# Kernel optimization log

Measured on AMD Instinct MI355X. Metric: run time of the kernel, lower is better.

Reference implementation:

```python
import jax, jax.numpy as jnp
import numpy as np

B, S, D, H = 1, 2048, 2048, 16
NOPE, ROPE, VH = 128, 64, 128
QK = NOPE + ROPE
QLORA, KVLORA = 1536, 512


def rms_norm(x, w, eps=1e-6):
    xf = x.astype(jnp.float32)
    y = xf * jax.lax.rsqrt(jnp.mean(xf * xf, axis=-1, keepdims=True) + eps)
    return (w * y).astype(x.dtype)


def apply_rope(x, cos, sin):
    # x: [b, s, h, d]; cos/sin: [s, d/2]; complex mult on consecutive pairs
    x2 = x.reshape(*x.shape[:-1], -1, 2)
    x0, x1 = x2[..., 0], x2[..., 1]
    c = cos[None, :, None, :]
    s = sin[None, :, None, :]
    y0 = x0 * c - x1 * s
    y1 = x0 * s + x1 * c
    return jnp.stack([y0, y1], axis=-1).reshape(x.shape).astype(x.dtype)


def setup_inputs() -> dict:
    key = jax.random.key(0)
    ks = jax.random.split(key, 8)
    init = lambda k, shape, fan: (jax.random.normal(k, shape, jnp.float32) / np.sqrt(fan))
    x = jax.random.normal(ks[0], (B, S, D), jnp.float32)
    wq_down_w = init(ks[1], (QLORA, D), D)
    wq_down_b = jnp.zeros((QLORA,), jnp.float32)
    q_norm_w = jnp.ones((QLORA,), jnp.float32)
    wq_up_w = init(ks[2], (H * QK, QLORA), QLORA)
    wq_up_b = jnp.zeros((H * QK,), jnp.float32)
    wkv_down_w = init(ks[3], (KVLORA + ROPE, D), D)
    wkv_down_b = jnp.zeros((KVLORA + ROPE,), jnp.float32)
    kv_norm_w = jnp.ones((KVLORA,), jnp.float32)
    wkv_up_w = init(ks[4], (H * (NOPE + VH), KVLORA), KVLORA)
    wkv_up_b = jnp.zeros((H * (NOPE + VH),), jnp.float32)
    wo_w = init(ks[5], (D, H * VH), H * VH)
    wo_b = jnp.zeros((D,), jnp.float32)
    pos = jnp.arange(S, dtype=jnp.float32)
    inv = 1.0 / (10000.0 ** (jnp.arange(0, ROPE, 2, dtype=jnp.float32) / ROPE))
    ang = pos[:, None] * inv[None, :]  # [S, ROPE/2]
    freqs_cos, freqs_sin = jnp.cos(ang), jnp.sin(ang)
    causal = jnp.tril(jnp.ones((S, S), bool))
    mask = jnp.broadcast_to(jnp.where(causal, 0.0, -1e9).astype(jnp.float32), (B, S, S))
    return dict(x=x, start_pos=0, freqs_cos=freqs_cos, freqs_sin=freqs_sin, mask=mask,
                wq_down_w=wq_down_w, wq_down_b=wq_down_b, q_norm_w=q_norm_w,
                wq_up_w=wq_up_w, wq_up_b=wq_up_b,
                wkv_down_w=wkv_down_w, wkv_down_b=wkv_down_b, kv_norm_w=kv_norm_w,
                wkv_up_w=wkv_up_w, wkv_up_b=wkv_up_b, wo_w=wo_w, wo_b=wo_b)


def reference(x, start_pos, freqs_cos, freqs_sin, mask,
              wq_down_w, wq_down_b, q_norm_w, wq_up_w, wq_up_b,
              wkv_down_w, wkv_down_b, kv_norm_w, wkv_up_w, wkv_up_b,
              wo_w, wo_b):
    bsz, seqlen, _ = x.shape
    scale = QK ** (-0.5)
    # low-rank query path
    q = rms_norm(x @ wq_down_w.T + wq_down_b, q_norm_w)
    q = (q @ wq_up_w.T + wq_up_b).reshape(bsz, seqlen, H, QK)
    q_nope, q_pe = q[..., :NOPE], q[..., NOPE:]
    q_pe = apply_rope(q_pe, freqs_cos, freqs_sin)
    # low-rank kv path with decoupled rope key
    kv = x @ wkv_down_w.T + wkv_down_b
    kv_lat, k_pe = kv[..., :KVLORA], kv[..., KVLORA:]
    kv_up = rms_norm(kv_lat, kv_norm_w) @ wkv_up_w.T + wkv_up_b
    kv_up = kv_up.reshape(bsz, seqlen, H, NOPE + VH)
    k_nope, v = kv_up[..., :NOPE], kv_up[..., NOPE:]
    k_pe = apply_rope(k_pe[:, :, None, :], freqs_cos, freqs_sin)  # [b,s,1,ROPE]
    qf = jnp.concatenate([q_nope, q_pe], axis=-1)
    kf = jnp.concatenate([k_nope, jnp.broadcast_to(k_pe, (bsz, seqlen, H, ROPE))], axis=-1)
    scores = jnp.einsum('bqhd,bkhd->bhqk', qf, kf) * scale
    scores = scores + mask[:, None, :, :]
    probs = jax.nn.softmax(scores.astype(jnp.float32), axis=-1).astype(x.dtype)
    out = jnp.einsum('bhqk,bkhd->bqhd', probs, v).reshape(bsz, seqlen, H * VH)
    return out @ wo_w.T + wo_b
```

## Files before the change

### kernel.cpp

```cpp
#include <hip/hip_runtime.h>
#include <math.h>

typedef __attribute__((ext_vector_type(8))) __bf16 bf16x8;
typedef __attribute__((ext_vector_type(8))) short short8;
typedef __attribute__((ext_vector_type(4))) float f32x4;
typedef __attribute__((ext_vector_type(4))) unsigned short u16x4;

#define S_LEN 2048
#define NHEAD 16

__device__ __forceinline__ unsigned short f2b(float f) {
    unsigned int u = __float_as_uint(f);
    u = (u + 0x7fffu + ((u >> 16) & 1u)) >> 16;
    return (unsigned short)u;
}

__device__ __forceinline__ f32x4 mfma16(short8 a, short8 b, f32x4 c) {
    return __builtin_amdgcn_mfma_f32_16x16x32_bf16(
        __builtin_bit_cast(bf16x8, a), __builtin_bit_cast(bf16x8, b), c, 0, 0, 0);
}

#define GLDS(gptr, lptr)                                                              \
    __builtin_amdgcn_global_load_lds(                                                 \
        (const __attribute__((address_space(1))) unsigned int*)(gptr),                \
        (__attribute__((address_space(3))) unsigned int*)(lptr), 16, 0, 0)

__global__ __launch_bounds__(256) void cvt_f2b(const float* __restrict__ in,
                                               unsigned short* __restrict__ out, int n4) {
    int i = blockIdx.x * 256 + threadIdx.x;
    if (i >= n4) return;
    float4 v = ((const float4*)in)[i];
    u16x4 o;
    o[0] = f2b(v.x); o[1] = f2b(v.y); o[2] = f2b(v.z); o[3] = f2b(v.w);
    ((u16x4*)out)[i] = o;
}

__global__ __launch_bounds__(256) void cvt_f2b_pad(const float* __restrict__ in,
                                                   unsigned short* __restrict__ out,
                                                   int N, int K, int Npad) {
    int i = blockIdx.x * 256 + threadIdx.x;
    int total4 = Npad * (K >> 2);
    if (i >= total4) return;
    int r = (i * 4) / K;
    u16x4 o = {0, 0, 0, 0};
    if (r < N) {
        float4 v = ((const float4*)in)[i];
        o[0] = f2b(v.x); o[1] = f2b(v.y); o[2] = f2b(v.z); o[3] = f2b(v.w);
    }
    ((u16x4*)out)[i] = o;
}

__global__ __launch_bounds__(256) void gemm_bt(const unsigned short* __restrict__ A,
                                               const unsigned short* __restrict__ W,
                                               const float* __restrict__ bias,
                                               float* __restrict__ C,
                                               int M, int N, int K, int Npad,
                                               int tiles_m) {
    __shared__ __align__(16) unsigned short sA[128 * 32];
    __shared__ __align__(16) unsigned short sB[128 * 32];
    const int tid = threadIdx.x;
    const int wave = tid >> 6, lane = tid & 63;
    const int l15 = lane & 15, l4 = lane >> 4;
    const int wm = wave >> 1, wn = wave & 1;

    const int nwg = gridDim.x;
    const int q8 = nwg >> 3, r8 = nwg & 7;
    const int xcd = blockIdx.x & 7, ii = blockIdx.x >> 3;
    const int sw = ((xcd < r8) ? xcd * (q8 + 1) : r8 * (q8 + 1) + (xcd - r8) * q8) + ii;
    const int bm = sw % tiles_m, bn = sw / tiles_m;

    f32x4 acc[4][4] = {};
    const int nkt = K >> 5;
    for (int kt = 0; kt < nkt; ++kt) {
#pragma unroll
        for (int j = 0; j < 2; ++j) {
            int cbase = (j * 4 + wave) * 64;
            int c = cbase + lane;
            int r = c >> 2, c8 = c & 3;
            GLDS(&A[(size_t)(bm * 128 + r) * K + kt * 32 + c8 * 8],
                 (char*)sA + cbase * 16);
            GLDS(&W[(size_t)(bn * 128 + r) * K + kt * 32 + c8 * 8],
                 (char*)sB + cbase * 16);
        }
        __syncthreads();
        short8 af[4], bf[4];
#pragma unroll
        for (int mi = 0; mi < 4; ++mi)
            af[mi] = *(const short8*)&sA[(wm * 64 + mi * 16 + l15) * 32 + 8 * l4];
#pragma unroll
        for (int ni = 0; ni < 4; ++ni)
            bf[ni] = *(const short8*)&sB[(wn * 64 + ni * 16 + l15) * 32 + 8 * l4];
#pragma unroll
        for (int mi = 0; mi < 4; ++mi)
#pragma unroll
            for (int ni = 0; ni < 4; ++ni)
                acc[mi][ni] = mfma16(af[mi], bf[ni], acc[mi][ni]);
        __syncthreads();
    }
#pragma unroll
    for (int mi = 0; mi < 4; ++mi) {
        int row = bm * 128 + wm * 64 + mi * 16 + 4 * l4;
#pragma unroll
        for (int ni = 0; ni < 4; ++ni) {
            int col = bn * 128 + wn * 64 + ni * 16 + l15;
            float b = (col < N) ? bias[col] : 0.f;
#pragma unroll
            for (int r = 0; r < 4; ++r)
                C[(size_t)(row + r) * Npad + col] = acc[mi][ni][r] + b;
        }
    }
}

__global__ __launch_bounds__(256) void rmsnorm_k(const float* __restrict__ in,
                                                 const float* __restrict__ w,
                                                 unsigned short* __restrict__ out,
                                                 int K, int ldin) {
    int row = blockIdx.x, tid = threadIdx.x;
    const float* p = in + (size_t)row * ldin;
    float ss = 0.f;
    for (int i = tid; i < K; i += 256) { float v = p[i]; ss += v * v; }
#pragma unroll
    for (int off = 1; off < 64; off <<= 1) ss += __shfl_xor(ss, off, 64);
    __shared__ float red[4];
    if ((tid & 63) == 0) red[tid >> 6] = ss;
    __syncthreads();
    float tot = red[0] + red[1] + red[2] + red[3];
    float rinv = rsqrtf(tot / (float)K + 1e-6f);
    for (int i = tid; i < K; i += 256)
        out[(size_t)row * K + i] = f2b(p[i] * rinv * w[i]);
}

__global__ __launch_bounds__(256) void assemble_q(const float* __restrict__ qup,
                                                  const float* __restrict__ fcos,
                                                  const float* __restrict__ fsin,
                                                  unsigned short* __restrict__ qf) {
    int s = blockIdx.x, tid = threadIdx.x;
    const float scale = 0.07216878365f;
    for (int idx = tid; idx < NHEAD * 128; idx += 256) {
        int h = idx >> 7, j = idx & 127;
        qf[((size_t)h * S_LEN + s) * 192 + j] = f2b(qup[(size_t)s * 3072 + h * 192 + j] * scale);
    }
    for (int idx = tid; idx < NHEAD * 32; idx += 256) {
        int h = idx >> 5, j = idx & 31;
        float x0 = qup[(size_t)s * 3072 + h * 192 + 128 + 2 * j];
        float x1 = qup[(size_t)s * 3072 + h * 192 + 128 + 2 * j + 1];
        float c = fcos[s * 32 + j], sn = fsin[s * 32 + j];
        size_t base = ((size_t)h * S_LEN + s) * 192 + 128 + 2 * j;
        qf[base]     = f2b((x0 * c - x1 * sn) * scale);
        qf[base + 1] = f2b((x0 * sn + x1 * c) * scale);
    }
}

__global__ __launch_bounds__(256) void assemble_k(const float* __restrict__ kvup,
                                                  const float* __restrict__ kvd,
                                                  const float* __restrict__ fcos,
                                                  const float* __restrict__ fsin,
                                                  unsigned short* __restrict__ kf) {
    int s = blockIdx.x, tid = threadIdx.x;
    __shared__ unsigned short pe[64];
    if (tid < 32) {
        int j = tid;
        float x0 = kvd[(size_t)s * 640 + 512 + 2 * j];
        float x1 = kvd[(size_t)s * 640 + 512 + 2 * j + 1];
        float c = fcos[s * 32 + j], sn = fsin[s * 32 + j];
        pe[2 * j]     = f2b(x0 * c - x1 * sn);
        pe[2 * j + 1] = f2b(x0 * sn + x1 * c);
    }
    __syncthreads();
    for (int idx = tid; idx < NHEAD * 128; idx += 256) {
        int h = idx >> 7, j = idx & 127;
        kf[((size_t)h * S_LEN + s) * 192 + j] = f2b(kvup[(size_t)s * 4096 + h * 256 + j]);
    }
    for (int idx = tid; idx < NHEAD * 64; idx += 256) {
        int h = idx >> 6, j = idx & 63;
        kf[((size_t)h * S_LEN + s) * 192 + 128 + j] = pe[j];
    }
}

__global__ __launch_bounds__(256) void assemble_v(const float* __restrict__ kvup,
                                                  unsigned short* __restrict__ vT) {
    __shared__ unsigned short t[64][136];
    int sb = blockIdx.x, h = blockIdx.y, tid = threadIdx.x;
#pragma unroll
    for (int i = 0; i < 8; ++i) {
        int idx = tid + i * 256;
        int s = idx >> 5, c4 = idx & 31;
        float4 v = *(const float4*)&kvup[(size_t)(sb * 64 + s) * 4096 + h * 256 + 128 + c4 * 4];
        t[s][c4 * 4 + 0] = f2b(v.x); t[s][c4 * 4 + 1] = f2b(v.y);
        t[s][c4 * 4 + 2] = f2b(v.z); t[s][c4 * 4 + 3] = f2b(v.w);
    }
    __syncthreads();
#pragma unroll
    for (int i = 0; i < 4; ++i) {
        int idx = tid + i * 256;
        int d = idx >> 3, s8 = idx & 7;
        short8 o;
#pragma unroll
        for (int j = 0; j < 8; ++j) o[j] = t[s8 * 8 + j][d];
        *(short8*)&vT[((size_t)h * 128 + d) * S_LEN + sb * 64 + s8 * 8] = o;
    }
}

__global__ __launch_bounds__(256) void flash_attn(const unsigned short* __restrict__ qf,
                                                  const unsigned short* __restrict__ kf,
                                                  const unsigned short* __restrict__ vT,
                                                  unsigned short* __restrict__ attn) {
    __shared__ __align__(16) unsigned short sK[64 * 192];
    __shared__ __align__(16) unsigned short sV[128 * 64];
    __shared__ __align__(16) unsigned short sP[4 * 16 * 64];
    const int tid = threadIdx.x;
    const int wave = tid >> 6, lane = tid & 63;
    const int l15 = lane & 15, l4 = lane >> 4;
    const int bid = blockIdx.x;
    const int h = bid & 15, iph = bid >> 4;
    const int qb = (iph < 16) ? iph : 47 - iph;

    const unsigned short* kbase = kf + (size_t)h * S_LEN * 192;
    const unsigned short* vbase = vT + (size_t)h * 128 * S_LEN;

    int ksrc[6];
#pragma unroll
    for (int i = 0; i < 6; ++i) {
        int c = i * 256 + tid, r = c / 24, c8 = c % 24;
        ksrc[i] = r * 192 + (c8 ^ (r & 7)) * 8;
    }
    int vsrc[4];
#pragma unroll
    for (int i = 0; i < 4; ++i) {
        int c = i * 256 + tid, d = c >> 3, k8 = c & 7;
        vsrc[i] = d * S_LEN + (k8 ^ (d & 7)) * 8;
    }

    short8 qfrag[6];
    {
        const unsigned short* qp =
            qf + ((size_t)h * S_LEN + qb * 64 + wave * 16 + l15) * 192 + 8 * l4;
#pragma unroll
        for (int ks = 0; ks < 6; ++ks) qfrag[ks] = *(const short8*)(qp + ks * 32);
    }
    f32x4 oacc[8] = {};
    float m_r[4] = {-INFINITY, -INFINITY, -INFINITY, -INFINITY};
    float l_r[4] = {0.f, 0.f, 0.f, 0.f};

    for (int kb = 0; kb <= qb; ++kb) {
        const unsigned short* kt = kbase + (size_t)kb * 64 * 192;
        const unsigned short* vt = vbase + (size_t)kb * 64;
#pragma unroll
        for (int i = 0; i < 6; ++i)
            GLDS(kt + ksrc[i], (char*)sK + (i * 256 + wave * 64) * 16);
#pragma unroll
        for (int i = 0; i < 4; ++i)
            GLDS(vt + vsrc[i], (char*)sV + (i * 256 + wave * 64) * 16);
        __syncthreads();

        f32x4 sc[4] = {};
#pragma unroll
        for (int ks = 0; ks < 6; ++ks)
#pragma unroll
            for (int ni = 0; ni < 4; ++ni) {
                int r = ni * 16 + l15;
                short8 bfr = *(const short8*)((char*)sK + r * 384 + (((ks * 4 + l4) ^ (r & 7)) * 16));
                sc[ni] = mfma16(qfrag[ks], bfr, sc[ni]);
            }

        const bool diag = (kb == qb);
        float p[4][4], alpha[4];
#pragma unroll
        for (int r = 0; r < 4; ++r) {
            int qrow = wave * 16 + 4 * l4 + r;
            float mx = -1e30f;
#pragma unroll
            for (int ni = 0; ni < 4; ++ni) {
                float sv = sc[ni][r];
                if (diag && (ni * 16 + l15 > qrow)) sv = -1e30f;
                p[ni][r] = sv;
                mx = fmaxf(mx, sv);
            }
#pragma unroll
            for (int off = 1; off < 16; off <<= 1) mx = fmaxf(mx, __shfl_xor(mx, off, 16));
            float mnew = fmaxf(m_r[r], mx);
            alpha[r] = __expf(m_r[r] - mnew);
            float rs = 0.f;
#pragma unroll
            for (int ni = 0; ni < 4; ++ni) {
                float pe = __expf(p[ni][r] - mnew);
                p[ni][r] = pe;
                rs += pe;
            }
#pragma unroll
            for (int off = 1; off < 16; off <<= 1) rs += __shfl_xor(rs, off, 16);
            l_r[r] = l_r[r] * alpha[r] + rs;
            m_r[r] = mnew;
        }
#pragma unroll
        for (int ni2 = 0; ni2 < 8; ++ni2)
#pragma unroll
            for (int r = 0; r < 4; ++r) oacc[ni2][r] *= alpha[r];
#pragma unroll
        for (int ni = 0; ni < 4; ++ni)
#pragma unroll
            for (int r = 0; r < 4; ++r) {
                int prow = 4 * l4 + r;
                int pbyte = wave * 2048 + ((prow * 128 + (ni * 16 + l15) * 2) ^ ((prow & 7) << 4));
                *(unsigned short*)((char*)sP + pbyte) = f2b(p[ni][r]);
            }
#pragma unroll
        for (int ks2 = 0; ks2 < 2; ++ks2) {
            short8 pa = *(const short8*)((char*)sP + wave * 2048 + l15 * 128 +
                                         (((ks2 * 4 + l4) ^ (l15 & 7)) * 16));
#pragma unroll
            for (int ni2 = 0; ni2 < 8; ++ni2) {
                int d = ni2 * 16 + l15;
                short8 vb = *(const short8*)((char*)sV + d * 128 +
                                             (((ks2 * 4 + l4) ^ (d & 7)) * 16));
                oacc[ni2] = mfma16(pa, vb, oacc[ni2]);
            }
        }
        __syncthreads();
    }
#pragma unroll
    for (int ni2 = 0; ni2 < 8; ++ni2) {
        int col = h * 128 + ni2 * 16 + l15;
#pragma unroll
        for (int r = 0; r < 4; ++r) {
            int row = qb * 64 + wave * 16 + 4 * l4 + r;
            attn[(size_t)row * 2048 + col] = f2b(oacc[ni2][r] / l_r[r]);
        }
    }
}

extern "C" void kernel_launch(void* const* d_in, const int* in_sizes, int n_in,
                              void* d_out, int out_size, void* d_ws, size_t ws_size,
                              hipStream_t stream) {
    (void)in_sizes; (void)n_in; (void)out_size; (void)ws_size;
    const float* x    = (const float*)d_in[0];
    const float* fcos = (const float*)d_in[2];
    const float* fsin = (const float*)d_in[3];
    const float* wqd  = (const float*)d_in[5];
    const float* bqd  = (const float*)d_in[6];
    const float* qnw  = (const float*)d_in[7];
    const float* wqu  = (const float*)d_in[8];
    const float* bqu  = (const float*)d_in[9];
    const float* wkvd = (const float*)d_in[10];
    const float* bkvd = (const float*)d_in[11];
    const float* kvnw = (const float*)d_in[12];
    const float* wkvu = (const float*)d_in[13];
    const float* bkvu = (const float*)d_in[14];
    const float* wo   = (const float*)d_in[15];
    const float* bwo  = (const float*)d_in[16];
    float* out = (float*)d_out;

    char* ws = (char*)d_ws;
    size_t off = 0;
    auto alloc = [&](size_t bytes) {
        void* p = ws + off;
        off += (bytes + 255) & ~(size_t)255;
        return p;
    };
    unsigned short* xb     = (unsigned short*)alloc(2048ull * 2048 * 2);
    unsigned short* wqd16  = (unsigned short*)alloc(1536ull * 2048 * 2);
    unsigned short* wqu16  = (unsigned short*)alloc(3072ull * 1536 * 2);
    unsigned short* wkvd16 = (unsigned short*)alloc(640ull * 2048 * 2);
    unsigned short* wkvu16 = (unsigned short*)alloc(4096ull * 512 * 2);
    char* slotA            = (char*)alloc(2048ull * 3072 * 4);
    unsigned short* qn16   = (unsigned short*)alloc(2048ull * 1536 * 2);
    unsigned short* qf16   = (unsigned short*)alloc(16ull * 2048 * 192 * 2);
    float* kvd32           = (float*)alloc(2048ull * 640 * 4);
    unsigned short* kvn16  = (unsigned short*)alloc(2048ull * 512 * 2);
    char* slotB            = (char*)alloc(2048ull * 4096 * 4);
    unsigned short* kf16   = (unsigned short*)alloc(16ull * 2048 * 192 * 2);
    unsigned short* vT16   = (unsigned short*)alloc(16ull * 128 * 2048 * 2);

    float* qdown32 = (float*)slotA;
    float* qup32   = (float*)slotA;
    unsigned short* attn16 = (unsigned short*)slotA;
    float* kvup32  = (float*)slotB;
    unsigned short* wo16 = (unsigned short*)slotB;

    cvt_f2b<<<4096, 256, 0, stream>>>(x, xb, 2048 * 2048 / 4);
    cvt_f2b<<<3072, 256, 0, stream>>>(wqd, wqd16, 1536 * 2048 / 4);
    cvt_f2b<<<4608, 256, 0, stream>>>(wqu, wqu16, 3072 * 1536 / 4);
    cvt_f2b_pad<<<1280, 256, 0, stream>>>(wkvd, wkvd16, 576, 2048, 640);
    cvt_f2b<<<2048, 256, 0, stream>>>(wkvu, wkvu16, 4096 * 512 / 4);

    gemm_bt<<<16 * 12, 256, 0, stream>>>(xb, wqd16, bqd, qdown32, 2048, 1536, 2048, 1536, 16);
    rmsnorm_k<<<2048, 256, 0, stream>>>(qdown32, qnw, qn16, 1536, 1536);
    gemm_bt<<<16 * 24, 256, 0, stream>>>(qn16, wqu16, bqu, qup32, 2048, 3072, 1536, 3072, 16);

    gemm_bt<<<16 * 5, 256, 0, stream>>>(xb, wkvd16, bkvd, kvd32, 2048, 576, 2048, 640, 16);
    rmsnorm_k<<<2048, 256, 0, stream>>>(kvd32, kvnw, kvn16, 512, 640);
    gemm_bt<<<16 * 32, 256, 0, stream>>>(kvn16, wkvu16, bkvu, kvup32, 2048, 4096, 512, 4096, 16);

    assemble_q<<<2048, 256, 0, stream>>>(qup32, fcos, fsin, qf16);
    assemble_k<<<2048, 256, 0, stream>>>(kvup32, kvd32, fcos, fsin, kf16);
    assemble_v<<<dim3(32, 16), 256, 0, stream>>>(kvup32, vT16);

    cvt_f2b<<<4096, 256, 0, stream>>>(wo, wo16, 2048 * 2048 / 4);

    flash_attn<<<512, 256, 0, stream>>>(qf16, kf16, vT16, attn16);
    gemm_bt<<<16 * 16, 256, 0, stream>>>(attn16, wo16, bwo, out, 2048, 2048, 2048, 2048, 16);
}
```

Baseline: 489.8 us.

## Double-buffer LDS tiles in GEMM and flash attention to overlap loads

Both the GEMM and the flash-attention kernels now use two LDS buffers. The next tile is prefetched with global_load_lds while the current tile is consumed by MFMAs, and each loop iteration keeps only one barrier. The GEMM K-tile also grows from 32 to 64 with two MFMA sub-steps per tile. This targets exposed global-load latency and halves the barrier count, at the cost of more LDS per block, which may reduce occupancy. Correctness relies on the single barrier at the end of each iteration covering the async LDS writes; there is no explicit vmcnt wait before the next tile is read.

```diff
diff --git a/kernel.cpp b/kernel.cpp
--- a/kernel.cpp
+++ b/kernel.cpp
@@ -56,8 +56,8 @@
                                                float* __restrict__ C,
                                                int M, int N, int K, int Npad,
                                                int tiles_m) {
-    __shared__ __align__(16) unsigned short sA[128 * 32];
-    __shared__ __align__(16) unsigned short sB[128 * 32];
+    __shared__ __align__(16) unsigned short sA[2][128 * 64];
+    __shared__ __align__(16) unsigned short sB[2][128 * 64];
     const int tid = threadIdx.x;
     const int wave = tid >> 6, lane = tid & 63;
     const int l15 = lane & 15, l4 = lane >> 4;
@@ -69,32 +69,47 @@
     const int sw = ((xcd < r8) ? xcd * (q8 + 1) : r8 * (q8 + 1) + (xcd - r8) * q8) + ii;
     const int bm = sw % tiles_m, bn = sw / tiles_m;
 
+    const unsigned short* Abase = A + (size_t)bm * 128 * K;
+    const unsigned short* Wbase = W + (size_t)bn * 128 * K;
+    int srcoff[4];
+#pragma unroll
+    for (int j = 0; j < 4; ++j) {
+        int c = j * 256 + tid;
+        srcoff[j] = (c >> 3) * K + (c & 7) * 8;
+    }
+
+    auto STAGE = [&](int kt, int buf) {
+#pragma unroll
+        for (int j = 0; j < 4; ++j) {
+            GLDS(Abase + kt * 64 + srcoff[j], (char*)sA[buf] + (j * 256 + wave * 64) * 16);
+            GLDS(Wbase + kt * 64 + srcoff[j], (char*)sB[buf] + (j * 256 + wave * 64) * 16);
+        }
+    };
+
     f32x4 acc[4][4] = {};
-    const int nkt = K >> 5;
+    const int nkt = K >> 6;
+    STAGE(0, 0);
+    __syncthreads();
     for (int kt = 0; kt < nkt; ++kt) {
-#pragma unroll
-        for (int j = 0; j < 2; ++j) {
-            int cbase = (j * 4 + wave) * 64;
-            int c = cbase + lane;
-            int r = c >> 2, c8 = c & 3;
-            GLDS(&A[(size_t)(bm * 128 + r) * K + kt * 32 + c8 * 8],
-                 (char*)sA + cbase * 16);
-            GLDS(&W[(size_t)(bn * 128 + r) * K + kt * 32 + c8 * 8],
-                 (char*)sB + cbase * 16);
-        }
-        __syncthreads();
-        short8 af[4], bf[4];
-#pragma unroll
-        for (int mi = 0; mi < 4; ++mi)
-            af[mi] = *(const short8*)&sA[(wm * 64 + mi * 16 + l15) * 32 + 8 * l4];
-#pragma unroll
-        for (int ni = 0; ni < 4; ++ni)
-            bf[ni] = *(const short8*)&sB[(wn * 64 + ni * 16 + l15) * 32 + 8 * l4];
-#pragma unroll
-        for (int mi = 0; mi < 4; ++mi)
+        const int cur = kt & 1;
+        if (kt + 1 < nkt) STAGE(kt + 1, cur ^ 1);
+        const unsigned short* pA = sA[cur];
+        const unsigned short* pB = sB[cur];
+#pragma unroll
+        for (int ks = 0; ks < 2; ++ks) {
+            short8 af[4], bf[4];
+#pragma unroll
+            for (int mi = 0; mi < 4; ++mi)
+                af[mi] = *(const short8*)&pA[(wm * 64 + mi * 16 + l15) * 64 + ks * 32 + 8 * l4];
 #pragma unroll
             for (int ni = 0; ni < 4; ++ni)
-                acc[mi][ni] = mfma16(af[mi], bf[ni], acc[mi][ni]);
+                bf[ni] = *(const short8*)&pB[(wn * 64 + ni * 16 + l15) * 64 + ks * 32 + 8 * l4];
+#pragma unroll
+            for (int mi = 0; mi < 4; ++mi)
+#pragma unroll
+                for (int ni = 0; ni < 4; ++ni)
+                    acc[mi][ni] = mfma16(af[mi], bf[ni], acc[mi][ni]);
+        }
         __syncthreads();
     }
 #pragma unroll
@@ -205,8 +220,8 @@
                                                   const unsigned short* __restrict__ kf,
                                                   const unsigned short* __restrict__ vT,
                                                   unsigned short* __restrict__ attn) {
-    __shared__ __align__(16) unsigned short sK[64 * 192];
-    __shared__ __align__(16) unsigned short sV[128 * 64];
+    __shared__ __align__(16) unsigned short sK[2][64 * 192];
+    __shared__ __align__(16) unsigned short sV[2][128 * 64];
     __shared__ __align__(16) unsigned short sP[4 * 16 * 64];
     const int tid = threadIdx.x;
     const int wave = tid >> 6, lane = tid & 63;
@@ -231,6 +246,17 @@
         vsrc[i] = d * S_LEN + (k8 ^ (d & 7)) * 8;
     }
 
+    auto STAGE = [&](int kb, int buf) {
+        const unsigned short* kt = kbase + (size_t)kb * 64 * 192;
+        const unsigned short* vt = vbase + (size_t)kb * 64;
+#pragma unroll
+        for (int i = 0; i < 6; ++i)
+            GLDS(kt + ksrc[i], (char*)sK[buf] + (i * 256 + wave * 64) * 16);
+#pragma unroll
+        for (int i = 0; i < 4; ++i)
+            GLDS(vt + vsrc[i], (char*)sV[buf] + (i * 256 + wave * 64) * 16);
+    };
+
     short8 qfrag[6];
     {
         const unsigned short* qp =
@@ -242,16 +268,13 @@
     float m_r[4] = {-INFINITY, -INFINITY, -INFINITY, -INFINITY};
     float l_r[4] = {0.f, 0.f, 0.f, 0.f};
 
+    STAGE(0, 0);
+    __syncthreads();
     for (int kb = 0; kb <= qb; ++kb) {
-        const unsigned short* kt = kbase + (size_t)kb * 64 * 192;
-        const unsigned short* vt = vbase + (size_t)kb * 64;
-#pragma unroll
-        for (int i = 0; i < 6; ++i)
-            GLDS(kt + ksrc[i], (char*)sK + (i * 256 + wave * 64) * 16);
-#pragma unroll
-        for (int i = 0; i < 4; ++i)
-            GLDS(vt + vsrc[i], (char*)sV + (i * 256 + wave * 64) * 16);
-        __syncthreads();
+        const int cur = kb & 1;
+        if (kb < qb) STAGE(kb + 1, cur ^ 1);
+        const char* pK = (const char*)sK[cur];
+        const char* pV = (const char*)sV[cur];
 
         f32x4 sc[4] = {};
 #pragma unroll
@@ -259,7 +282,7 @@
 #pragma unroll
             for (int ni = 0; ni < 4; ++ni) {
                 int r = ni * 16 + l15;
-                short8 bfr = *(const short8*)((char*)sK + r * 384 + (((ks * 4 + l4) ^ (r & 7)) * 16));
+                short8 bfr = *(const short8*)(pK + r * 384 + (((ks * 4 + l4) ^ (r & 7)) * 16));
                 sc[ni] = mfma16(qfrag[ks], bfr, sc[ni]);
             }
 
@@ -311,8 +334,7 @@
 #pragma unroll
             for (int ni2 = 0; ni2 < 8; ++ni2) {
                 int d = ni2 * 16 + l15;
-                short8 vb = *(const short8*)((char*)sV + d * 128 +
-                                             (((ks2 * 4 + l4) ^ (d & 7)) * 16));
+                short8 vb = *(const short8*)(pV + d * 128 + (((ks2 * 4 + l4) ^ (d & 7)) * 16));
                 oacc[ni2] = mfma16(pa, vb, oacc[ni2]);
             }
         }
```

After: 460.6 us. 1.06x faster.
